# Performance work log

Measured on AMD Instinct MI355X. Metric: run time of the kernel, lower is better.

## Reference

```python
import jax, jax.numpy as jnp
import numpy as np

N_NODES = 75000
N_EDGES = 1200000
DIM = 64


def setup_inputs() -> dict:
    key = jax.random.key(0)
    ks = jax.random.split(key, 9)
    d_u = jax.random.normal(ks[0], (N_NODES, DIM), dtype=jnp.float32)
    p_u = jax.random.normal(ks[1], (N_NODES, DIM), dtype=jnp.float32)
    s = 1.0 / np.sqrt(DIM)
    w_q = jax.random.normal(ks[2], (DIM, DIM), dtype=jnp.float32) * s
    w_k = jax.random.normal(ks[3], (DIM, DIM), dtype=jnp.float32) * s
    w_v = jax.random.normal(ks[4], (DIM, DIM), dtype=jnp.float32) * s
    e1 = jax.random.normal(ks[5], (DIM,), dtype=jnp.float32) * s
    e2 = jax.random.normal(ks[6], (DIM,), dtype=jnp.float32) * s
    src = jax.random.randint(ks[7], (N_EDGES,), 0, N_NODES, dtype=jnp.int32)
    dst = jax.random.randint(ks[8], (N_EDGES,), 0, N_NODES, dtype=jnp.int32)
    return {"d_u": d_u, "p_u": p_u, "w_q": w_q, "w_k": w_k, "w_v": w_v,
            "e1": e1, "e2": e2, "src": src, "dst": dst}


def reference(d_u, p_u, w_q, w_k, w_v, e1, e2, src, dst):
    n_nodes = d_u.shape[0]
    # per-node edge scores: e1(w_k(p_u)) on src side, e2(w_q(d_u)) on dst side
    h_src = (p_u @ w_k.T) @ e1            # [N]
    h_dst = (d_u @ w_q.T) @ e2            # [N]
    # apply_edges(u_add_v): c_e = h_src[u] + h_dst[v], shape [E]
    c = h_src[src] + h_dst[dst]
    # EdgeWeightNorm(norm='right'): divide by sum of incoming edge weights at dst
    denom = jax.ops.segment_sum(c, dst, num_segments=n_nodes)  # [N]
    c = c / denom[dst]
    # update_all(u_mul_e, sum): messages w_v(p_u)[u] * c_e, summed at dst
    wv = p_u @ w_v.T                      # [N, D]
    msg = wv[src] * c[:, None]            # [E, D]
    out = jax.ops.segment_sum(msg, dst, num_segments=n_nodes)  # [N, D]
    return out
```

## Files before the change

### kernel.cpp

```cpp
#include <hip/hip_runtime.h>

#define N_NODES 75000
#define N_EDGES 1200000
#define DIM 64
#define SCAN_BLK 1024
#define N_SCAN_BLKS ((N_NODES + SCAN_BLK - 1) / SCAN_BLK)

__device__ __forceinline__ float lane_bc(float v, int l) {
    return __int_as_float(__builtin_amdgcn_readlane(__float_as_int(v), l));
}

__global__ void vec_precompute(const float* __restrict__ w_q,
                               const float* __restrict__ w_k,
                               const float* __restrict__ e1,
                               const float* __restrict__ e2,
                               double* __restrict__ a,
                               double* __restrict__ b) {
    int t = threadIdx.x;
    if (t < DIM) {
        double s = 0.0;
        #pragma unroll
        for (int j = 0; j < DIM; ++j) s += (double)e1[j] * (double)w_k[j * DIM + t];
        a[t] = s;
    } else if (t < 2 * DIM) {
        int d = t - DIM;
        double s = 0.0;
        #pragma unroll
        for (int j = 0; j < DIM; ++j) s += (double)e2[j] * (double)w_q[j * DIM + d];
        b[d] = s;
    }
}

__global__ __launch_bounds__(256, 4) void node_wave(
    const float* __restrict__ d_u, const float* __restrict__ p_u,
    const float* __restrict__ w_v,
    const double* __restrict__ a_vec, const double* __restrict__ b_vec,
    double* __restrict__ h_src, double* __restrict__ h_dst,
    float* __restrict__ wv_out) {
    int lane = threadIdx.x & 63;
    int wave = (blockIdx.x * 256 + threadIdx.x) >> 6;
    int nwaves = gridDim.x * 4;

    float w[DIM];
    const float4* wr = (const float4*)(w_v + (size_t)lane * DIM);
    #pragma unroll
    for (int k = 0; k < DIM / 4; ++k) {
        float4 v = wr[k];
        w[4 * k + 0] = v.x; w[4 * k + 1] = v.y;
        w[4 * k + 2] = v.z; w[4 * k + 3] = v.w;
    }
    double al = a_vec[lane];
    double bl = b_vec[lane];

    for (int i = wave; i < N_NODES; i += nwaves) {
        float pl = p_u[(size_t)i * DIM + lane];
        float dl = d_u[(size_t)i * DIM + lane];

        double hs = (double)pl * al;
        #pragma unroll
        for (int off = 32; off > 0; off >>= 1) hs += __shfl_xor(hs, off, 64);
        double hd = (double)dl * bl;
        #pragma unroll
        for (int off = 32; off > 0; off >>= 1) hd += __shfl_xor(hd, off, 64);
        if (lane == 0) { h_src[i] = hs; h_dst[i] = hd; }

        float a0 = 0.f, a1 = 0.f, a2 = 0.f, a3 = 0.f;
        #pragma unroll
        for (int d = 0; d < DIM; d += 4) {
            a0 += w[d + 0] * lane_bc(pl, d + 0);
            a1 += w[d + 1] * lane_bc(pl, d + 1);
            a2 += w[d + 2] * lane_bc(pl, d + 2);
            a3 += w[d + 3] * lane_bc(pl, d + 3);
        }
        wv_out[(size_t)i * DIM + lane] = (a0 + a1) + (a2 + a3);
    }
}

__global__ __launch_bounds__(256) void hist_kernel(
    const int* __restrict__ dst, int* __restrict__ cnt,
    int* __restrict__ rank) {
    int e = blockIdx.x * 256 + threadIdx.x;
    if (e >= N_EDGES) return;
    rank[e] = atomicAdd(&cnt[dst[e]], 1);
}

__global__ __launch_bounds__(SCAN_BLK) void scan1_kernel(
    const int* __restrict__ cnt, int* __restrict__ row,
    int* __restrict__ bsum) {
    __shared__ int sh[SCAN_BLK];
    int tid = threadIdx.x;
    int i = blockIdx.x * SCAN_BLK + tid;
    int v = (i < N_NODES) ? cnt[i] : 0;
    sh[tid] = v;
    __syncthreads();
    for (int off = 1; off < SCAN_BLK; off <<= 1) {
        int t = (tid >= off) ? sh[tid - off] : 0;
        __syncthreads();
        sh[tid] += t;
        __syncthreads();
    }
    if (i < N_NODES) row[i] = sh[tid] - v;
    if (tid == SCAN_BLK - 1) bsum[blockIdx.x] = sh[tid];
}

__global__ __launch_bounds__(256) void scan23_kernel(
    int* __restrict__ row, const int* __restrict__ bsum) {
    __shared__ int pref[N_SCAN_BLKS];
    int tid = threadIdx.x;
    if (tid == 0) {
        int run = 0;
        #pragma unroll 8
        for (int k = 0; k < N_SCAN_BLKS; ++k) { pref[k] = run; run += bsum[k]; }
    }
    __syncthreads();
    int i = blockIdx.x * 256 + tid;
    if (i >= N_NODES) return;
    row[i] += pref[i / SCAN_BLK];
}

__global__ __launch_bounds__(256) void build_kernel(
    const int* __restrict__ src, const int* __restrict__ dst,
    const int* __restrict__ row, const int* __restrict__ rank,
    int* __restrict__ csr_src) {
    int e = blockIdx.x * 256 + threadIdx.x;
    if (e >= N_EDGES) return;
    int pos = row[dst[e]] + rank[e];
    csr_src[pos] = src[e];
}

__global__ __launch_bounds__(256) void node_gather(
    const int* __restrict__ row, const int* __restrict__ cnt,
    const int* __restrict__ csr_src,
    const double* __restrict__ h_src, const double* __restrict__ h_dst,
    const float* __restrict__ wv, float* __restrict__ out) {
    int gtid = blockIdx.x * 256 + threadIdx.x;
    int node = gtid >> 6;
    int lane = threadIdx.x & 63;
    if (node >= N_NODES) return;

    int start = row[node];
    int deg = cnt[node];
    double hd = h_dst[node];

    if (deg <= 64) {
        int s0 = 0;
        double c0 = 0.0;
        if (lane < deg) {
            s0 = csr_src[start + lane];
            c0 = h_src[s0] + hd;
        }
        double r = c0;
        #pragma unroll
        for (int off = 32; off > 0; off >>= 1) r += __shfl_xor(r, off, 64);
        double inv = 1.0 / r;
        float cf0 = (lane < deg) ? (float)(c0 * inv) : 0.f;

        int g = lane >> 4;
        int q = lane & 15;
        int tmax = (deg + 3) >> 2;
        float ax = 0.f, ay = 0.f, az = 0.f, aw = 0.f;
        for (int t = 0; t < tmax; ++t) {
            int idx = 4 * t + g;
            int s = __shfl(s0, idx, 64);
            float cf = __shfl(cf0, idx, 64);
            const float4* rowp = (const float4*)(wv + (size_t)s * DIM);
            float4 w = rowp[q];
            ax += w.x * cf;
            ay += w.y * cf;
            az += w.z * cf;
            aw += w.w * cf;
        }
        ax += __shfl_xor(ax, 16, 64);
        ay += __shfl_xor(ay, 16, 64);
        az += __shfl_xor(az, 16, 64);
        aw += __shfl_xor(aw, 16, 64);
        ax += __shfl_xor(ax, 32, 64);
        ay += __shfl_xor(ay, 32, 64);
        az += __shfl_xor(az, 32, 64);
        aw += __shfl_xor(aw, 32, 64);
        if (lane < 16) {
            float4 st; st.x = ax; st.y = ay; st.z = az; st.w = aw;
            ((float4*)(out + (size_t)node * DIM))[q] = st;
        }
    } else {
        double denom = 0.0;
        for (int base = 0; base < deg; base += 64) {
            int m = deg - base; if (m > 64) m = 64;
            double c = 0.0;
            if (lane < m) {
                int s = csr_src[start + base + lane];
                c = h_src[s] + hd;
            }
            #pragma unroll
            for (int off = 32; off > 0; off >>= 1) c += __shfl_xor(c, off, 64);
            denom += c;
        }
        double inv = 1.0 / denom;
        float acc = 0.f;
        for (int base = 0; base < deg; base += 64) {
            int m = deg - base; if (m > 64) m = 64;
            int s1 = 0; float cf1 = 0.f;
            if (lane < m) {
                s1 = csr_src[start + base + lane];
                cf1 = (float)((h_src[s1] + hd) * inv);
            }
            for (int j = 0; j < m; ++j) {
                int s = __shfl(s1, j, 64);
                float cf = __shfl(cf1, j, 64);
                acc += wv[(size_t)s * DIM + lane] * cf;
            }
        }
        out[(size_t)node * DIM + lane] = acc;
    }
}

extern "C" void kernel_launch(void* const* d_in, const int* in_sizes, int n_in,
                              void* d_out, int out_size, void* d_ws, size_t ws_size,
                              hipStream_t stream) {
    const float* d_u = (const float*)d_in[0];
    const float* p_u = (const float*)d_in[1];
    const float* w_q = (const float*)d_in[2];
    const float* w_k = (const float*)d_in[3];
    const float* w_v = (const float*)d_in[4];
    const float* e1  = (const float*)d_in[5];
    const float* e2  = (const float*)d_in[6];
    const int*   src = (const int*)d_in[7];
    const int*   dst = (const int*)d_in[8];
    float* out = (float*)d_out;

    double* a      = (double*)d_ws;
    double* b      = a + DIM;
    double* h_src  = b + DIM;
    double* h_dst  = h_src + N_NODES;
    float*  wv     = (float*)(h_dst + N_NODES);
    int*    cnt    = (int*)(wv + (size_t)N_NODES * DIM);
    int*    row    = cnt + N_NODES;
    int*    bsum   = row + N_NODES;
    int*    rank   = bsum + 128;
    int*    csr_src= rank + N_EDGES;

    vec_precompute<<<1, 128, 0, stream>>>(w_q, w_k, e1, e2, a, b);

    hipMemsetAsync(cnt, 0, sizeof(int) * N_NODES, stream);

    hist_kernel<<<(N_EDGES + 255) / 256, 256, 0, stream>>>(dst, cnt, rank);

    node_wave<<<1024, 256, 0, stream>>>(
        d_u, p_u, w_v, a, b, h_src, h_dst, wv);

    scan1_kernel<<<N_SCAN_BLKS, SCAN_BLK, 0, stream>>>(cnt, row, bsum);
    scan23_kernel<<<(N_NODES + 255) / 256, 256, 0, stream>>>(row, bsum);

    build_kernel<<<(N_EDGES + 255) / 256, 256, 0, stream>>>(
        src, dst, row, rank, csr_src);

    node_gather<<<(N_NODES * 64 + 255) / 256, 256, 0, stream>>>(
        row, cnt, csr_src, h_src, h_dst, wv, out);
}
```

Before: 259.0 us.

## Use readlane broadcasts in gather and multi-edge threads in hist/build

The low-degree gather path now assigns one lane per feature. Each source row is read as a coalesced 256-byte line, and the edge index and coefficient come from scalar readlane broadcasts rather than shuffles. This replaces the float4 four-group layout and removes its final cross-group reductions. The hist and build kernels each process several edges per thread using grid-stride loops with fixed block counts, which cuts block launch overhead. The trade-off is more serial iterations per wave in the gather, one edge per load, against fewer shuffles.

```diff
diff --git a/kernel.cpp b/kernel.cpp
--- a/kernel.cpp
+++ b/kernel.cpp
@@ -6,8 +6,11 @@
 #define SCAN_BLK 1024
 #define N_SCAN_BLKS ((N_NODES + SCAN_BLK - 1) / SCAN_BLK)
 
-__device__ __forceinline__ float lane_bc(float v, int l) {
+__device__ __forceinline__ float lane_bcf(float v, int l) {
     return __int_as_float(__builtin_amdgcn_readlane(__float_as_int(v), l));
+}
+__device__ __forceinline__ int lane_bci(int v, int l) {
+    return __builtin_amdgcn_readlane(v, l);
 }
 
 __global__ void vec_precompute(const float* __restrict__ w_q,
@@ -67,21 +70,26 @@
         float a0 = 0.f, a1 = 0.f, a2 = 0.f, a3 = 0.f;
         #pragma unroll
         for (int d = 0; d < DIM; d += 4) {
-            a0 += w[d + 0] * lane_bc(pl, d + 0);
-            a1 += w[d + 1] * lane_bc(pl, d + 1);
-            a2 += w[d + 2] * lane_bc(pl, d + 2);
-            a3 += w[d + 3] * lane_bc(pl, d + 3);
+            a0 += w[d + 0] * lane_bcf(pl, d + 0);
+            a1 += w[d + 1] * lane_bcf(pl, d + 1);
+            a2 += w[d + 2] * lane_bcf(pl, d + 2);
+            a3 += w[d + 3] * lane_bcf(pl, d + 3);
         }
         wv_out[(size_t)i * DIM + lane] = (a0 + a1) + (a2 + a3);
     }
 }
 
+#define HIST_BLKS 1172
 __global__ __launch_bounds__(256) void hist_kernel(
     const int* __restrict__ dst, int* __restrict__ cnt,
     int* __restrict__ rank) {
-    int e = blockIdx.x * 256 + threadIdx.x;
-    if (e >= N_EDGES) return;
-    rank[e] = atomicAdd(&cnt[dst[e]], 1);
+    int t = blockIdx.x * 256 + threadIdx.x;
+    const int T = HIST_BLKS * 256;
+    #pragma unroll
+    for (int k = 0; k < 4; ++k) {
+        int e = t + k * T;
+        if (e < N_EDGES) rank[e] = atomicAdd(&cnt[dst[e]], 1);
+    }
 }
 
 __global__ __launch_bounds__(SCAN_BLK) void scan1_kernel(
@@ -118,14 +126,21 @@
     row[i] += pref[i / SCAN_BLK];
 }
 
+#define BUILD_BLKS 2344
 __global__ __launch_bounds__(256) void build_kernel(
     const int* __restrict__ src, const int* __restrict__ dst,
     const int* __restrict__ row, const int* __restrict__ rank,
     int* __restrict__ csr_src) {
-    int e = blockIdx.x * 256 + threadIdx.x;
-    if (e >= N_EDGES) return;
-    int pos = row[dst[e]] + rank[e];
-    csr_src[pos] = src[e];
+    int t = blockIdx.x * 256 + threadIdx.x;
+    const int T = BUILD_BLKS * 256;
+    #pragma unroll
+    for (int k = 0; k < 2; ++k) {
+        int e = t + k * T;
+        if (e < N_EDGES) {
+            int pos = row[dst[e]] + rank[e];
+            csr_src[pos] = src[e];
+        }
+    }
 }
 
 __global__ __launch_bounds__(256) void node_gather(
@@ -155,33 +170,27 @@
         double inv = 1.0 / r;
         float cf0 = (lane < deg) ? (float)(c0 * inv) : 0.f;
 
-        int g = lane >> 4;
-        int q = lane & 15;
-        int tmax = (deg + 3) >> 2;
-        float ax = 0.f, ay = 0.f, az = 0.f, aw = 0.f;
-        for (int t = 0; t < tmax; ++t) {
-            int idx = 4 * t + g;
-            int s = __shfl(s0, idx, 64);
-            float cf = __shfl(cf0, idx, 64);
-            const float4* rowp = (const float4*)(wv + (size_t)s * DIM);
-            float4 w = rowp[q];
-            ax += w.x * cf;
-            ay += w.y * cf;
-            az += w.z * cf;
-            aw += w.w * cf;
-        }
-        ax += __shfl_xor(ax, 16, 64);
-        ay += __shfl_xor(ay, 16, 64);
-        az += __shfl_xor(az, 16, 64);
-        aw += __shfl_xor(aw, 16, 64);
-        ax += __shfl_xor(ax, 32, 64);
-        ay += __shfl_xor(ay, 32, 64);
-        az += __shfl_xor(az, 32, 64);
-        aw += __shfl_xor(aw, 32, 64);
-        if (lane < 16) {
-            float4 st; st.x = ax; st.y = ay; st.z = az; st.w = aw;
-            ((float4*)(out + (size_t)node * DIM))[q] = st;
-        }
+        float acc = 0.f;
+        int j = 0;
+        for (; j + 4 <= deg; j += 4) {
+            int sA = lane_bci(s0, j + 0); float cA = lane_bcf(cf0, j + 0);
+            int sB = lane_bci(s0, j + 1); float cB = lane_bcf(cf0, j + 1);
+            int sC = lane_bci(s0, j + 2); float cC = lane_bcf(cf0, j + 2);
+            int sD = lane_bci(s0, j + 3); float cD = lane_bcf(cf0, j + 3);
+            float wA = wv[(size_t)sA * DIM + lane];
+            float wB = wv[(size_t)sB * DIM + lane];
+            float wC = wv[(size_t)sC * DIM + lane];
+            float wD = wv[(size_t)sD * DIM + lane];
+            acc += wA * cA;
+            acc += wB * cB;
+            acc += wC * cC;
+            acc += wD * cD;
+        }
+        for (; j < deg; ++j) {
+            int s = lane_bci(s0, j); float cf = lane_bcf(cf0, j);
+            acc += wv[(size_t)s * DIM + lane] * cf;
+        }
+        out[(size_t)node * DIM + lane] = acc;
     } else {
         double denom = 0.0;
         for (int base = 0; base < deg; base += 64) {
@@ -205,8 +214,8 @@
                 cf1 = (float)((h_src[s1] + hd) * inv);
             }
             for (int j = 0; j < m; ++j) {
-                int s = __shfl(s1, j, 64);
-                float cf = __shfl(cf1, j, 64);
+                int s = lane_bci(s1, j);
+                float cf = lane_bcf(cf1, j);
                 acc += wv[(size_t)s * DIM + lane] * cf;
             }
         }
@@ -243,7 +252,7 @@
 
     hipMemsetAsync(cnt, 0, sizeof(int) * N_NODES, stream);
 
-    hist_kernel<<<(N_EDGES + 255) / 256, 256, 0, stream>>>(dst, cnt, rank);
+    hist_kernel<<<HIST_BLKS, 256, 0, stream>>>(dst, cnt, rank);
 
     node_wave<<<1024, 256, 0, stream>>>(
         d_u, p_u, w_v, a, b, h_src, h_dst, wv);
@@ -251,7 +260,7 @@
     scan1_kernel<<<N_SCAN_BLKS, SCAN_BLK, 0, stream>>>(cnt, row, bsum);
     scan23_kernel<<<(N_NODES + 255) / 256, 256, 0, stream>>>(row, bsum);
 
-    build_kernel<<<(N_EDGES + 255) / 256, 256, 0, stream>>>(
+    build_kernel<<<BUILD_BLKS, 256, 0, stream>>>(
         src, dst, row, rank, csr_src);
 
     node_gather<<<(N_NODES * 64 + 255) / 256, 256, 0, stream>>>(
```

Measured after the change: 267.3 us. 3.2% more time.
